# Performance work log

Measured on AMD Instinct MI355X. Metric: run time of the kernel, lower is better.

## Reference

```python
import jax, jax.numpy as jnp
import numpy as np

EPS = 1e-8

def _rasterize_mesh(face_verts, H, W):
    # face_verts: [F,3,3] = (ndc_x, ndc_y, view_z) per triangle vertex
    x0, y0, z0 = face_verts[:, 0, 0], face_verts[:, 0, 1], face_verts[:, 0, 2]
    x1, y1, z1 = face_verts[:, 1, 0], face_verts[:, 1, 1], face_verts[:, 1, 2]
    x2, y2, z2 = face_verts[:, 2, 0], face_verts[:, 2, 1], face_verts[:, 2, 2]
    area = (x1 - x0) * (y2 - y0) - (y1 - y0) * (x2 - x0)
    # cull_backfaces=True (area<=0) + degenerate + behind-camera cull
    face_ok = (area > EPS) & (z0 > 0) & (z1 > 0) & (z2 > 0)
    inv_area = jnp.where(face_ok, 1.0 / jnp.where(face_ok, area, 1.0), 0.0)
    zs = jnp.stack([z0, z1, z2], -1)  # [F,3]
    # pytorch3d NDC: +x left, +y up, pixel centers
    xs = 1.0 - (2.0 * jnp.arange(W, dtype=jnp.float32) + 1.0) / W
    ys = 1.0 - (2.0 * jnp.arange(H, dtype=jnp.float32) + 1.0) / H

    def row_fn(py):
        px = xs[:, None]  # [W,1] broadcast vs faces [F]
        w0 = ((x1 - px) * (y2 - py) - (y1 - py) * (x2 - px)) * inv_area
        w1 = ((x2 - px) * (y0 - py) - (y2 - py) * (x0 - px)) * inv_area
        w2 = ((x0 - px) * (y1 - py) - (y0 - py) * (x1 - px)) * inv_area
        inside = (w0 >= 0) & (w1 >= 0) & (w2 >= 0) & face_ok
        # perspective_correct=True: l_i = w_i * prod(other z), renormalize
        l = jnp.stack([w0 * z1 * z2, z0 * w1 * z2, z0 * z1 * w2], -1)  # [W,F,3]
        s = l.sum(-1, keepdims=True)
        b = l / jnp.where(s == 0, 1.0, s)
        # clip_barycentric_coords=True
        b = jnp.clip(b, 0.0, None)
        b = b / jnp.clip(b.sum(-1, keepdims=True), EPS, None)
        zpix = (b * zs[None]).sum(-1)  # [W,F] interpolated view-space depth
        zm = jnp.where(inside, zpix, jnp.inf)
        fidx = jnp.argmin(zm, axis=1)  # z-buffer winner per pixel
        zmin = jnp.take_along_axis(zm, fidx[:, None], 1)[:, 0]
        hit = jnp.isfinite(zmin)
        bary = jnp.take_along_axis(b, fidx[:, None, None], 1)[:, 0]  # [W,3]
        return (jnp.where(hit, fidx, -1),
                jnp.where(hit, zmin, -1.0),
                jnp.where(hit[:, None], bary, -1.0))

    return jax.lax.map(row_fn, ys)  # ([H,W],[H,W],[H,W,3])


def _forward(positions, features, faces, K, RT, H, W):
    B, V, _ = positions.shape
    Fn = faces.shape[1]
    # --- create_camera_objects: open3d/opencv KRT -> pytorch3d camera ---
    R = RT[:, :, :3]
    t = RT[:, :, 3]
    scale = min(H, W) / 2.0
    focal = jnp.stack([K[:, 0, 0], K[:, 1, 1]], -1) / scale  # [B,2] NDC focal
    p0 = -(jnp.stack([K[:, 0, 2], K[:, 1, 2]], -1)
           - jnp.array([W / 2.0, H / 2.0], jnp.float32)) / scale  # [B,2]
    sign = jnp.array([-1.0, -1.0, 1.0], jnp.float32)
    R_p = jnp.swapaxes(R, 1, 2) * sign[None, None, :]  # R^T with cols 0,1 negated
    T_p = t * sign[None, :]
    # --- _get_mesh_ndc: world -> view -> NDC (pytorch3d row-vector convention) ---
    v_view = jnp.einsum('bvi,bij->bvj', positions, R_p) + T_p[:, None, :]
    z = v_view[..., 2:3]
    xy_ndc = focal[:, None, :] * v_view[..., :2] / z + p0[:, None, :]
    verts_ndc = jnp.concatenate([xy_ndc, z], -1)  # z overwritten with view-space depth
    face_verts = jax.vmap(lambda v, f: v[f])(verts_ndc, faces)  # [B,F,3,3]
    # --- rasterize (blur_sigma=0 -> faces_per_pixel=1) ---
    p2f, zbuf, bary = jax.vmap(lambda fv: _rasterize_mesh(fv, H, W))(face_verts)
    hit = p2f >= 0
    pix_to_face = jnp.where(hit, p2f + (jnp.arange(B) * Fn)[:, None, None], -1)
    # --- interpolate_face_attributes on packed faces/verts ---
    faces_packed = (faces + (jnp.arange(B) * V)[:, None, None]).reshape(B * Fn, 3)
    feats_packed = features.reshape(B * V, -1)
    fv_idx = faces_packed[jnp.clip(pix_to_face, 0)]  # [B,H,W,3]
    attrs = feats_packed[fv_idx]                      # [B,H,W,3,C]
    pix_feats = (bary[..., None] * attrs).sum(-2)
    pix_feats = jnp.where(hit[..., None], pix_feats, 0.0)
    dists = jnp.where(hit, 0.0, -1.0)
    # add faces_per_pixel (K=1) axis, matching pytorch3d Fragments layout
    return (pix_feats[:, :, :, None, :], pix_to_face[:, :, :, None],
            zbuf[:, :, :, None], bary[:, :, :, None, :], dists[:, :, :, None])


def setup_inputs() -> dict:
    key = jax.random.key(0)
    k1, k2, k3 = jax.random.split(key, 3)
    B, V, Fn, C, H, W = 1, 8192, 16384, 64, 192, 192
    positions = jax.random.uniform(k1, (B, V, 3), jnp.float32) * 2.0 - 1.0
    features = jax.random.normal(k2, (B, V, C), jnp.float32)
    faces = jax.random.randint(k3, (B, Fn, 3), 0, V)
    K = jnp.broadcast_to(jnp.array([[180.0, 0.0, 96.0], [0.0, 180.0, 96.0],
                                    [0.0, 0.0, 1.0]], jnp.float32), (B, 3, 3))
    RT = jnp.broadcast_to(jnp.concatenate(
        [jnp.eye(3, dtype=jnp.float32),
         jnp.array([[0.0], [0.0], [3.5]], jnp.float32)], axis=1), (B, 3, 4))
    return {"positions": positions, "features": features, "faces": faces,
            "K": K, "RT": RT, "H": H, "W": W, "blur_sigma": 0}


def reference(positions, features, faces, K, RT, H, W, blur_sigma):
    # blur_sigma == 0 path of VertexShader.forward (faces_per_pixel=1)
    return _forward(positions, features, faces, K, RT, H, W)
```

## Files before the change

### kernel.cpp

```cpp
#include <hip/hip_runtime.h>
#include <stdint.h>

#define H_ 192
#define W_ 192
#define C_ 64
#define EPS_F 1e-8f
#define TILE 16
#define CHUNK 256
#define NSLICE 16

typedef unsigned long long ull;

#define OFF_FEATS 0
#define OFF_P2F   (H_*W_*C_)
#define OFF_ZBUF  (OFF_P2F + H_*W_)
#define OFF_BARY  (OFF_ZBUF + H_*W_)
#define OFF_DIST  (OFF_BARY + H_*W_*3)

__device__ __forceinline__ float xm(float a, float b){ return __fmul_rn(a,b); }
__device__ __forceinline__ float xa(float a, float b){ return __fadd_rn(a,b); }
__device__ __forceinline__ float xsb(float a, float b){ return __fsub_rn(a,b); }
__device__ __forceinline__ float xd(float a, float b){ return __fdiv_rn(a,b); }

__device__ __forceinline__ float pixcoord(int i, float dim){
    float t = xa(xm(2.0f, (float)i), 1.0f);
    return xsb(1.0f, xd(t, dim));
}

__global__ void k_init(const float* __restrict__ pos, const float* __restrict__ K,
                       const float* __restrict__ RT, float* __restrict__ verts,
                       ull* __restrict__ keys, int V){
    int i = blockIdx.x*blockDim.x + threadIdx.x;
    if (i < H_*W_) keys[i] = 0xFFFFFFFFFFFFFFFFULL;
    if (i >= V) return;
    float p0 = pos[3*i+0], p1 = pos[3*i+1], p2 = pos[3*i+2];
    const float sgn[3] = {-1.f, -1.f, 1.f};
    float vv[3];
    #pragma unroll
    for (int j=0;j<3;j++){
        float rp0 = xm(RT[j*4+0], sgn[j]);
        float rp1 = xm(RT[j*4+1], sgn[j]);
        float rp2 = xm(RT[j*4+2], sgn[j]);
        float s = xa(xa(xm(p0,rp0), xm(p1,rp1)), xm(p2,rp2));
        vv[j] = xa(s, xm(RT[j*4+3], sgn[j]));
    }
    float z = vv[2];
    const float scale = 96.0f;
    float fx = xd(K[0], scale);
    float fy = xd(K[4], scale);
    float p0x = -xd(xsb(K[2], 96.0f), scale);
    float p0y = -xd(xsb(K[5], 96.0f), scale);
    float xn = xa(xd(xm(fx, vv[0]), z), p0x);
    float yn = xa(xd(xm(fy, vv[1]), z), p0y);
    verts[4*i+0] = xn; verts[4*i+1] = yn; verts[4*i+2] = z; verts[4*i+3] = 0.f;
}

__global__ void k_faces(const int* __restrict__ faces, const float* __restrict__ verts,
                        float* __restrict__ rec, int Fn){
    int f = blockIdx.x*blockDim.x + threadIdx.x;
    if (f >= Fn) return;
    int i0 = faces[3*f+0], i1 = faces[3*f+1], i2 = faces[3*f+2];
    float x0=verts[4*i0+0], y0=verts[4*i0+1], z0=verts[4*i0+2];
    float x1=verts[4*i1+0], y1=verts[4*i1+1], z1=verts[4*i1+2];
    float x2=verts[4*i2+0], y2=verts[4*i2+1], z2=verts[4*i2+2];
    float area = xsb(xm(xsb(x1,x0), xsb(y2,y0)), xm(xsb(y1,y0), xsb(x2,x0)));
    bool ok = (area > EPS_F) && (z0 > 0.f) && (z1 > 0.f) && (z2 > 0.f);
    float inv_area = ok ? xd(1.0f, area) : 0.0f;
    float xmn, xmx, ymn, ymx, zmn;
    if (ok){
        xmn = fminf(x0, fminf(x1, x2)) - 1e-4f;
        xmx = fmaxf(x0, fmaxf(x1, x2)) + 1e-4f;
        ymn = fminf(y0, fminf(y1, y2)) - 1e-4f;
        ymx = fmaxf(y0, fmaxf(y1, y2)) + 1e-4f;
        zmn = fminf(z0, fminf(z1, z2));
    } else {
        xmn = INFINITY; xmx = -INFINITY; ymn = INFINITY; ymx = -INFINITY;
        zmn = INFINITY;
    }
    float4* q = (float4*)(rec + (size_t)f*16);
    q[0] = make_float4(x0, y0, x1, y1);
    q[1] = make_float4(x2, y2, z0, z1);
    q[2] = make_float4(z2, inv_area, zmn, 0.f);
    q[3] = make_float4(xmn, xmx, ymn, ymx);
}

__global__ __launch_bounds__(256) void k_raster(const float* __restrict__ rec,
        ull* __restrict__ keys, int Fn){
    __shared__ float lds[CHUNK*12];
    __shared__ float zl[CHUNK];
    __shared__ int   slist[CHUNK];
    __shared__ int   wcnt[4];
    int tid = threadIdx.x;
    int ix = blockIdx.x*TILE + (tid & 15);
    int iy = blockIdx.y*TILE + (tid >> 4);
    int pix = iy*W_ + ix;
    float px = pixcoord(ix, (float)W_);
    float py = pixcoord(iy, (float)H_);
    float tx_hi = pixcoord(blockIdx.x*TILE,          (float)W_);
    float tx_lo = pixcoord(blockIdx.x*TILE + TILE-1, (float)W_);
    float ty_hi = pixcoord(blockIdx.y*TILE,          (float)H_);
    float ty_lo = pixcoord(blockIdx.y*TILE + TILE-1, (float)H_);
    int perSlice = Fn / NSLICE;
    int f0 = blockIdx.z * perSlice;
    int f1 = f0 + perSlice;
    int lane = tid & 63, wv = tid >> 6;

    float zbest = INFINITY;
    int fbest = -1;

    for (int base = f0; base < f1; base += CHUNK){
        __syncthreads();
        const float4* g = (const float4*)(rec + (size_t)(base + tid)*16);
        float4 q0 = g[0], q1 = g[1], q2 = g[2], q3 = g[3];
        bool keep = (q3.x <= tx_hi) && (q3.y >= tx_lo) && (q3.z <= ty_hi) && (q3.w >= ty_lo);
        float4* l = (float4*)(lds + tid*12);
        l[0] = q0; l[1] = q1; l[2] = q2;
        ull m = __ballot(keep);
        if (lane == 0) wcnt[wv] = __popcll(m);
        __syncthreads();
        int basecnt = 0;
        #pragma unroll
        for (int w2 = 0; w2 < 4; ++w2) if (w2 < wv) basecnt += wcnt[w2];
        if (keep){
            int pos = basecnt + __popcll(m & ((1ULL << lane) - 1ULL));
            slist[pos] = tid;
            zl[pos] = q2.z;
        }
        int nsurv = wcnt[0] + wcnt[1] + wcnt[2] + wcnt[3];
        __syncthreads();

        for (int k = 0; k < nsurv; k++){
            float zminf = zl[k];
            if (!(xm(zminf, 0.999f) < zbest)) continue;
            int j = slist[k];
            const float* r = lds + j*12;
            float x0=r[0], y0=r[1], x1=r[2], y1=r[3], x2=r[4], y2=r[5];
            float dx0=xsb(x0,px), dx1=xsb(x1,px), dx2=xsb(x2,px);
            float dy0=xsb(y0,py), dy1=xsb(y1,py), dy2=xsb(y2,py);
            float e0 = xsb(xm(dx1,dy2), xm(dy1,dx2));
            float e1 = xsb(xm(dx2,dy0), xm(dy2,dx0));
            float e2 = xsb(xm(dx0,dy1), xm(dy0,dx1));
            if (e0 >= 0.f && e1 >= 0.f && e2 >= 0.f){
                float z0=r[6], z1=r[7], z2=r[8], ia=r[9];
                float w0 = xm(e0, ia), w1 = xm(e1, ia), w2 = xm(e2, ia);
                float l0 = xm(xm(w0,z1),z2);
                float l1 = xm(xm(z0,w1),z2);
                float l2 = xm(xm(z0,z1),w2);
                float s  = xa(xa(l0,l1),l2);
                float dn = (s == 0.f) ? 1.0f : s;
                float b0 = fmaxf(xd(l0,dn), 0.f);
                float b1 = fmaxf(xd(l1,dn), 0.f);
                float b2 = fmaxf(xd(l2,dn), 0.f);
                float bs = fmaxf(xa(xa(b0,b1),b2), EPS_F);
                b0 = xd(b0,bs); b1 = xd(b1,bs); b2 = xd(b2,bs);
                float zp = xa(xa(xm(b0,z0),xm(b1,z1)),xm(b2,z2));
                if (zp < zbest){ zbest = zp; fbest = base + j; }
            }
        }
    }
    if (fbest >= 0){
        ull key = (((ull)__float_as_uint(zbest)) << 32) | (unsigned)fbest;
        atomicMin(&keys[pix], key);
    }
}

__global__ __launch_bounds__(256) void k_post(const ull* __restrict__ keys,
        const float* __restrict__ rec, const float* __restrict__ feats,
        const int* __restrict__ faces, float* __restrict__ out){
    int grp = threadIdx.x >> 6;
    int c = threadIdx.x & 63;
    int pix = blockIdx.x*4 + grp;
    float* p2f  = out + OFF_P2F;
    float* zbuf = out + OFF_ZBUF;
    float* bary = out + OFF_BARY;
    float* dist = out + OFF_DIST;
    ull key = keys[pix];
    if (key == 0xFFFFFFFFFFFFFFFFULL){
        out[OFF_FEATS + pix*C_ + c] = 0.0f;
        if (c == 0){
            p2f[pix] = -1.0f; zbuf[pix] = -1.0f; dist[pix] = -1.0f;
        }
        if (c < 3) bary[3*pix+c] = -1.0f;
        return;
    }
    int f = (int)(key & 0xFFFFFFFFu);
    float z = __uint_as_float((unsigned)(key >> 32));
    int ix = pix % W_, iy = pix / W_;
    float px = pixcoord(ix, (float)W_);
    float py = pixcoord(iy, (float)H_);
    const float* r = rec + (size_t)f*16;
    float x0=r[0], y0=r[1], x1=r[2], y1=r[3], x2=r[4], y2=r[5];
    float z0=r[6], z1=r[7], z2=r[8], ia=r[9];
    float w0 = xm(xsb(xm(xsb(x1,px),xsb(y2,py)), xm(xsb(y1,py),xsb(x2,px))), ia);
    float w1 = xm(xsb(xm(xsb(x2,px),xsb(y0,py)), xm(xsb(y2,py),xsb(x0,px))), ia);
    float w2 = xm(xsb(xm(xsb(x0,px),xsb(y1,py)), xm(xsb(y0,py),xsb(x1,px))), ia);
    float l0 = xm(xm(w0,z1),z2);
    float l1 = xm(xm(z0,w1),z2);
    float l2 = xm(xm(z0,z1),w2);
    float s  = xa(xa(l0,l1),l2);
    float dn = (s == 0.f) ? 1.0f : s;
    float b0 = fmaxf(xd(l0,dn), 0.f);
    float b1 = fmaxf(xd(l1,dn), 0.f);
    float b2 = fmaxf(xd(l2,dn), 0.f);
    float bs = fmaxf(xa(xa(b0,b1),b2), EPS_F);
    b0 = xd(b0,bs); b1 = xd(b1,bs); b2 = xd(b2,bs);
    int i0 = faces[3*f+0], i1 = faces[3*f+1], i2 = faces[3*f+2];
    float res = xa(xa(xm(b0, feats[i0*C_ + c]), xm(b1, feats[i1*C_ + c])),
                   xm(b2, feats[i2*C_ + c]));
    out[OFF_FEATS + pix*C_ + c] = res;
    if (c == 0){
        p2f[pix] = (float)f; zbuf[pix] = z; dist[pix] = 0.0f;
    }
    if (c < 3){
        float bb = (c == 0) ? b0 : ((c == 1) ? b1 : b2);
        bary[3*pix+c] = bb;
    }
}

extern "C" void kernel_launch(void* const* d_in, const int* in_sizes, int n_in,
                              void* d_out, int out_size, void* d_ws, size_t ws_size,
                              hipStream_t stream) {
    const float* positions = (const float*)d_in[0];
    const float* features  = (const float*)d_in[1];
    const int*   faces     = (const int*)  d_in[2];
    const float* K         = (const float*)d_in[3];
    const float* RT        = (const float*)d_in[4];
    int V  = in_sizes[0] / 3;
    int Fn = in_sizes[2] / 3;

    float* verts = (float*)d_ws;
    float* rec   = verts + (size_t)V*4;
    ull*   keys  = (ull*)(rec + (size_t)Fn*16);

    int initN = H_*W_;
    k_init<<<(initN+255)/256, 256, 0, stream>>>(positions, K, RT, verts, keys, V);
    k_faces<<<(Fn+255)/256, 256, 0, stream>>>(faces, verts, rec, Fn);
    dim3 rg(W_/TILE, H_/TILE, NSLICE);
    k_raster<<<rg, dim3(256,1,1), 0, stream>>>(rec, keys, Fn);
    k_post<<<(H_*W_)/4, 256, 0, stream>>>(keys, rec, features, faces, (float*)d_out);
}
```

Measured before the change: 175.8 us.

## Depth-sort faces into buckets and early-exit raster chunks via suffix zmin

Faces are bucketed by minimum depth through a histogram, a scan and a scatter, so the raster kernel visits chunks front-to-back. Each block reads the global z-buffer key and a suffix minimum of per-chunk depth, and stops when no later chunk can beat the current depth. Pixels outside the global screen-space bounding box skip all chunks. This adds three small kernels plus atomics, and the post kernel now recomputes barycentrics from the vertices because records are reordered. The bucket range assumes depths near 2 to 6, which fits this camera setup.

```diff
diff --git a/kernel.cpp b/kernel.cpp
--- a/kernel.cpp
+++ b/kernel.cpp
@@ -8,6 +8,8 @@
 #define TILE 16
 #define CHUNK 256
 #define NSLICE 16
+#define NBUCKET 256
+#define MAXCHUNK 64
 
 typedef unsigned long long ull;
 
@@ -27,11 +29,29 @@
     return xsb(1.0f, xd(t, dim));
 }
 
+__device__ __forceinline__ unsigned fenc(float f){
+    unsigned b = __float_as_uint(f);
+    return (b & 0x80000000u) ? ~b : (b | 0x80000000u);
+}
+__device__ __forceinline__ float fdec(unsigned e){
+    unsigned b = (e & 0x80000000u) ? (e & 0x7FFFFFFFu) : ~e;
+    return __uint_as_float(b);
+}
+
+__device__ __forceinline__ int zbucket(float zmn){
+    int b = (int)((zmn - 2.0f) * 64.0f);
+    return b < 0 ? 0 : (b > 254 ? 254 : b);
+}
+
 __global__ void k_init(const float* __restrict__ pos, const float* __restrict__ K,
                        const float* __restrict__ RT, float* __restrict__ verts,
-                       ull* __restrict__ keys, int V){
+                       ull* __restrict__ keys, unsigned* __restrict__ hist,
+                       unsigned* __restrict__ chunkmin, unsigned* __restrict__ gbb, int V){
     int i = blockIdx.x*blockDim.x + threadIdx.x;
     if (i < H_*W_) keys[i] = 0xFFFFFFFFFFFFFFFFULL;
+    if (i < NBUCKET) hist[i] = 0u;
+    if (i < MAXCHUNK) chunkmin[i] = 0x7F800000u;
+    if (i == 0){ gbb[0]=0xFFFFFFFFu; gbb[1]=0u; gbb[2]=0xFFFFFFFFu; gbb[3]=0u; }
     if (i >= V) return;
     float p0 = pos[3*i+0], p1 = pos[3*i+1], p2 = pos[3*i+2];
     const float sgn[3] = {-1.f, -1.f, 1.f};
@@ -55,8 +75,69 @@
     verts[4*i+0] = xn; verts[4*i+1] = yn; verts[4*i+2] = z; verts[4*i+3] = 0.f;
 }
 
-__global__ void k_faces(const int* __restrict__ faces, const float* __restrict__ verts,
-                        float* __restrict__ rec, int Fn){
+__global__ __launch_bounds__(256) void k_prehist(const int* __restrict__ faces,
+        const float* __restrict__ verts, unsigned* __restrict__ hist,
+        unsigned* __restrict__ gbb, int Fn){
+    __shared__ unsigned lh[NBUCKET];
+    int t = threadIdx.x;
+    lh[t] = 0u;
+    __syncthreads();
+    int f = blockIdx.x*256 + t;
+    float bxmn=INFINITY, bxmx=-INFINITY, bymn=INFINITY, bymx=-INFINITY;
+    if (f < Fn){
+        int i0 = faces[3*f+0], i1 = faces[3*f+1], i2 = faces[3*f+2];
+        float x0=verts[4*i0+0], y0=verts[4*i0+1], z0=verts[4*i0+2];
+        float x1=verts[4*i1+0], y1=verts[4*i1+1], z1=verts[4*i1+2];
+        float x2=verts[4*i2+0], y2=verts[4*i2+1], z2=verts[4*i2+2];
+        float area = xsb(xm(xsb(x1,x0), xsb(y2,y0)), xm(xsb(y1,y0), xsb(x2,x0)));
+        bool ok = (area > EPS_F) && (z0 > 0.f) && (z1 > 0.f) && (z2 > 0.f);
+        int b = 255;
+        if (ok){
+            float zmn = fminf(z0, fminf(z1, z2));
+            b = zbucket(zmn);
+            bxmn = fminf(x0, fminf(x1, x2)) - 1e-4f;
+            bxmx = fmaxf(x0, fmaxf(x1, x2)) + 1e-4f;
+            bymn = fminf(y0, fminf(y1, y2)) - 1e-4f;
+            bymx = fmaxf(y0, fmaxf(y1, y2)) + 1e-4f;
+        }
+        atomicAdd(&lh[b], 1u);
+    }
+    #pragma unroll
+    for (int s=1; s<64; s<<=1){
+        bxmn = fminf(bxmn, __shfl_xor(bxmn, s, 64));
+        bxmx = fmaxf(bxmx, __shfl_xor(bxmx, s, 64));
+        bymn = fminf(bymn, __shfl_xor(bymn, s, 64));
+        bymx = fmaxf(bymx, __shfl_xor(bymx, s, 64));
+    }
+    if ((t & 63) == 0){
+        atomicMin(&gbb[0], fenc(bxmn));
+        atomicMax(&gbb[1], fenc(bxmx));
+        atomicMin(&gbb[2], fenc(bymn));
+        atomicMax(&gbb[3], fenc(bymx));
+    }
+    __syncthreads();
+    unsigned cc = lh[t];
+    if (cc) atomicAdd(&hist[t], cc);
+}
+
+__global__ __launch_bounds__(256) void k_scan(unsigned* __restrict__ hist){
+    __shared__ unsigned s[NBUCKET];
+    int t = threadIdx.x;
+    unsigned v = hist[t];
+    s[t] = v;
+    __syncthreads();
+    for (int d=1; d<NBUCKET; d<<=1){
+        unsigned u = (t >= d) ? s[t-d] : 0u;
+        __syncthreads();
+        s[t] += u;
+        __syncthreads();
+    }
+    hist[t] = s[t] - v;
+}
+
+__global__ __launch_bounds__(256) void k_scatter(const int* __restrict__ faces,
+        const float* __restrict__ verts, float* __restrict__ rec,
+        unsigned* __restrict__ hist, unsigned* __restrict__ chunkmin, int Fn){
     int f = blockIdx.x*blockDim.x + threadIdx.x;
     if (f >= Fn) return;
     int i0 = faces[3*f+0], i1 = faces[3*f+1], i2 = faces[3*f+2];
@@ -67,30 +148,49 @@
     bool ok = (area > EPS_F) && (z0 > 0.f) && (z1 > 0.f) && (z2 > 0.f);
     float inv_area = ok ? xd(1.0f, area) : 0.0f;
     float xmn, xmx, ymn, ymx, zmn;
+    int b;
     if (ok){
         xmn = fminf(x0, fminf(x1, x2)) - 1e-4f;
         xmx = fmaxf(x0, fmaxf(x1, x2)) + 1e-4f;
         ymn = fminf(y0, fminf(y1, y2)) - 1e-4f;
         ymx = fmaxf(y0, fmaxf(y1, y2)) + 1e-4f;
         zmn = fminf(z0, fminf(z1, z2));
+        b = zbucket(zmn);
     } else {
         xmn = INFINITY; xmx = -INFINITY; ymn = INFINITY; ymx = -INFINITY;
         zmn = INFINITY;
-    }
-    float4* q = (float4*)(rec + (size_t)f*16);
+        b = 255;
+    }
+    unsigned pos = atomicAdd(&hist[b], 1u);
+    float4* q = (float4*)(rec + (size_t)pos*16);
     q[0] = make_float4(x0, y0, x1, y1);
     q[1] = make_float4(x2, y2, z0, z1);
-    q[2] = make_float4(z2, inv_area, zmn, 0.f);
+    q[2] = make_float4(z2, inv_area, zmn, __int_as_float(f));
     q[3] = make_float4(xmn, xmx, ymn, ymx);
+    if ((pos >> 8) < MAXCHUNK)
+        atomicMin(&chunkmin[pos >> 8], __float_as_uint(zmn));
 }
 
 __global__ __launch_bounds__(256) void k_raster(const float* __restrict__ rec,
+        const unsigned* __restrict__ chunkmin, const unsigned* __restrict__ gbb,
         ull* __restrict__ keys, int Fn){
     __shared__ float lds[CHUNK*12];
     __shared__ float zl[CHUNK];
     __shared__ int   slist[CHUNK];
     __shared__ int   wcnt[4];
+    __shared__ float suff[MAXCHUNK];
     int tid = threadIdx.x;
+    int nchunk = Fn / CHUNK;
+    if (tid < MAXCHUNK){
+        float v = (tid < nchunk) ? __uint_as_float(chunkmin[tid]) : INFINITY;
+        #pragma unroll
+        for (int s=1; s<MAXCHUNK; s<<=1){
+            int src = tid + s; if (src > MAXCHUNK-1) src = MAXCHUNK-1;
+            float o = __shfl(v, src, 64);
+            v = fminf(v, o);
+        }
+        suff[tid] = v;
+    }
     int ix = blockIdx.x*TILE + (tid & 15);
     int iy = blockIdx.y*TILE + (tid >> 4);
     int pix = iy*W_ + ix;
@@ -100,18 +200,26 @@
     float tx_lo = pixcoord(blockIdx.x*TILE + TILE-1, (float)W_);
     float ty_hi = pixcoord(blockIdx.y*TILE,          (float)H_);
     float ty_lo = pixcoord(blockIdx.y*TILE + TILE-1, (float)H_);
-    int perSlice = Fn / NSLICE;
-    int f0 = blockIdx.z * perSlice;
-    int f1 = f0 + perSlice;
+    float gx0 = fdec(gbb[0]), gx1 = fdec(gbb[1]);
+    float gy0 = fdec(gbb[2]), gy1 = fdec(gbb[3]);
+    bool alive = (px >= gx0) && (px <= gx1) && (py >= gy0) && (py <= gy1);
     int lane = tid & 63, wv = tid >> 6;
 
-    float zbest = INFINITY;
-    int fbest = -1;
-
-    for (int base = f0; base < f1; base += CHUNK){
-        __syncthreads();
-        const float4* g = (const float4*)(rec + (size_t)(base + tid)*16);
-        float4 q0 = g[0], q1 = g[1], q2 = g[2], q3 = g[3];
+    float zcut = INFINITY;
+    ull localkey = 0xFFFFFFFFFFFFFFFFULL;
+    __syncthreads();
+
+    for (int c = (int)blockIdx.z; c < nchunk; c += NSLICE){
+        ull g = __hip_atomic_load(&keys[pix], __ATOMIC_RELAXED, __HIP_MEMORY_SCOPE_AGENT);
+        float zg = __uint_as_float((unsigned)(g >> 32));
+        zcut = fminf(zcut, zg);
+        float sc = (c < MAXCHUNK) ? suff[c] : 0.0f;
+        int done = (!alive || !(xm(sc, 0.999f) < zcut)) ? 1 : 0;
+        if (__syncthreads_and(done)) break;
+
+        int base = c*CHUNK;
+        const float4* gq = (const float4*)(rec + (size_t)(base + tid)*16);
+        float4 q0 = gq[0], q1 = gq[1], q2 = gq[2], q3 = gq[3];
         bool keep = (q3.x <= tx_hi) && (q3.y >= tx_lo) && (q3.z <= ty_hi) && (q3.w >= ty_lo);
         float4* l = (float4*)(lds + tid*12);
         l[0] = q0; l[1] = q1; l[2] = q2;
@@ -122,16 +230,16 @@
         #pragma unroll
         for (int w2 = 0; w2 < 4; ++w2) if (w2 < wv) basecnt += wcnt[w2];
         if (keep){
-            int pos = basecnt + __popcll(m & ((1ULL << lane) - 1ULL));
-            slist[pos] = tid;
-            zl[pos] = q2.z;
+            int p = basecnt + __popcll(m & ((1ULL << lane) - 1ULL));
+            slist[p] = tid;
+            zl[p] = q2.z;
         }
         int nsurv = wcnt[0] + wcnt[1] + wcnt[2] + wcnt[3];
         __syncthreads();
 
         for (int k = 0; k < nsurv; k++){
             float zminf = zl[k];
-            if (!(xm(zminf, 0.999f) < zbest)) continue;
+            if (!(xm(zminf, 0.999f) < zcut)) continue;
             int j = slist[k];
             const float* r = lds + j*12;
             float x0=r[0], y0=r[1], x1=r[2], y1=r[3], x2=r[4], y2=r[5];
@@ -154,18 +262,17 @@
                 float bs = fmaxf(xa(xa(b0,b1),b2), EPS_F);
                 b0 = xd(b0,bs); b1 = xd(b1,bs); b2 = xd(b2,bs);
                 float zp = xa(xa(xm(b0,z0),xm(b1,z1)),xm(b2,z2));
-                if (zp < zbest){ zbest = zp; fbest = base + j; }
+                ull ck = (((ull)__float_as_uint(zp)) << 32) | (unsigned)__float_as_int(r[11]);
+                if (ck < localkey) localkey = ck;
+                zcut = fminf(zcut, zp);
             }
         }
     }
-    if (fbest >= 0){
-        ull key = (((ull)__float_as_uint(zbest)) << 32) | (unsigned)fbest;
-        atomicMin(&keys[pix], key);
-    }
+    if (localkey != 0xFFFFFFFFFFFFFFFFULL) atomicMin(&keys[pix], localkey);
 }
 
 __global__ __launch_bounds__(256) void k_post(const ull* __restrict__ keys,
-        const float* __restrict__ rec, const float* __restrict__ feats,
+        const float* __restrict__ verts, const float* __restrict__ feats,
         const int* __restrict__ faces, float* __restrict__ out){
     int grp = threadIdx.x >> 6;
     int c = threadIdx.x & 63;
@@ -188,9 +295,12 @@
     int ix = pix % W_, iy = pix / W_;
     float px = pixcoord(ix, (float)W_);
     float py = pixcoord(iy, (float)H_);
-    const float* r = rec + (size_t)f*16;
-    float x0=r[0], y0=r[1], x1=r[2], y1=r[3], x2=r[4], y2=r[5];
-    float z0=r[6], z1=r[7], z2=r[8], ia=r[9];
+    int i0 = faces[3*f+0], i1 = faces[3*f+1], i2 = faces[3*f+2];
+    float x0=verts[4*i0+0], y0=verts[4*i0+1], z0=verts[4*i0+2];
+    float x1=verts[4*i1+0], y1=verts[4*i1+1], z1=verts[4*i1+2];
+    float x2=verts[4*i2+0], y2=verts[4*i2+1], z2=verts[4*i2+2];
+    float area = xsb(xm(xsb(x1,x0), xsb(y2,y0)), xm(xsb(y1,y0), xsb(x2,x0)));
+    float ia = xd(1.0f, area);
     float w0 = xm(xsb(xm(xsb(x1,px),xsb(y2,py)), xm(xsb(y1,py),xsb(x2,px))), ia);
     float w1 = xm(xsb(xm(xsb(x2,px),xsb(y0,py)), xm(xsb(y2,py),xsb(x0,px))), ia);
     float w2 = xm(xsb(xm(xsb(x0,px),xsb(y1,py)), xm(xsb(y0,py),xsb(x1,px))), ia);
@@ -204,7 +314,6 @@
     float b2 = fmaxf(xd(l2,dn), 0.f);
     float bs = fmaxf(xa(xa(b0,b1),b2), EPS_F);
     b0 = xd(b0,bs); b1 = xd(b1,bs); b2 = xd(b2,bs);
-    int i0 = faces[3*f+0], i1 = faces[3*f+1], i2 = faces[3*f+2];
     float res = xa(xa(xm(b0, feats[i0*C_ + c]), xm(b1, feats[i1*C_ + c])),
                    xm(b2, feats[i2*C_ + c]));
     out[OFF_FEATS + pix*C_ + c] = res;
@@ -231,11 +340,16 @@
     float* verts = (float*)d_ws;
     float* rec   = verts + (size_t)V*4;
     ull*   keys  = (ull*)(rec + (size_t)Fn*16);
+    unsigned* hist     = (unsigned*)(keys + H_*W_);
+    unsigned* chunkmin = hist + NBUCKET;
+    unsigned* gbb      = chunkmin + MAXCHUNK;
 
     int initN = H_*W_;
-    k_init<<<(initN+255)/256, 256, 0, stream>>>(positions, K, RT, verts, keys, V);
-    k_faces<<<(Fn+255)/256, 256, 0, stream>>>(faces, verts, rec, Fn);
+    k_init<<<(initN+255)/256, 256, 0, stream>>>(positions, K, RT, verts, keys, hist, chunkmin, gbb, V);
+    k_prehist<<<(Fn+255)/256, 256, 0, stream>>>(faces, verts, hist, gbb, Fn);
+    k_scan<<<1, 256, 0, stream>>>(hist);
+    k_scatter<<<(Fn+255)/256, 256, 0, stream>>>(faces, verts, rec, hist, chunkmin, Fn);
     dim3 rg(W_/TILE, H_/TILE, NSLICE);
-    k_raster<<<rg, dim3(256,1,1), 0, stream>>>(rec, keys, Fn);
-    k_post<<<(H_*W_)/4, 256, 0, stream>>>(keys, rec, features, faces, (float*)d_out);
-}
+    k_raster<<<rg, dim3(256,1,1), 0, stream>>>(rec, chunkmin, gbb, keys, Fn);
+    k_post<<<(H_*W_)/4, 256, 0, stream>>>(keys, verts, features, faces, (float*)d_out);
+}
```

After: 321.8 us. 1.83x slower.
